# Performance work log

Hardware: AMD Instinct MI355X
Metric: run time of the kernel (lower is better)

Reference implementation:

```python
import jax, jax.numpy as jnp
import numpy as np

B, G, D = 16, 20000, 64   # batch, num_genes, feature_dim
S, L = 500, 128           # num_gene_sets, max genes per set (padded)


def setup_inputs() -> dict:
    key = jax.random.key(0)
    k1, k2, k3 = jax.random.split(key, 3)
    gene_features = jax.random.normal(k1, (B, G, D), dtype=jnp.float32)
    geneset_indices = jax.random.randint(k2, (S, L), 0, G, dtype=jnp.int32)
    set_mask = jnp.ones((S, L), dtype=bool)  # all positions valid (uniform-size sets)
    attn_weights = jax.random.normal(k3, (S, L, D), dtype=jnp.float32)
    return {
        "gene_features": gene_features,
        "attn_weights": attn_weights,
        "geneset_indices": geneset_indices,
        "set_mask": set_mask,
    }


def reference(gene_features, attn_weights, geneset_indices, set_mask):
    # Gather per-set gene features: [B, S, L, D]
    gathered = jnp.take(gene_features, geneset_indices, axis=1)
    # Masked softmax over the set-member axis L (independent per feature dim),
    # matching F.softmax(attention_weights, dim=1) per gene set.
    neg = jnp.finfo(attn_weights.dtype).min
    logits = jnp.where(set_mask[:, :, None], attn_weights, neg)  # [S, L, D]
    attn = jax.nn.softmax(logits, axis=1)                        # [S, L, D]
    # Weighted sum over set members -> [B, S, D]
    return jnp.einsum('bsld,sld->bsd', gathered, attn)
```

## Files before the change

kernel.cpp:

```cpp
#include <hip/hip_runtime.h>
#include <math.h>


#define NB 16
#define NG 20000
#define ND 64
#define NS 500
#define NL 128

__device__ __forceinline__ float bf2f(unsigned short u) {
    union { unsigned int i; float f; } x;
    x.i = ((unsigned int)u) << 16;
    return x.f;
}

__device__ __forceinline__ unsigned short f2bf(float f) {
    union { float f; unsigned int i; } x;
    x.f = f;
    unsigned int r = x.i + 0x7FFFu + ((x.i >> 16) & 1u);
    return (unsigned short)(r >> 16);
}

__global__ void detect_dtype_kernel(const unsigned short* __restrict__ aw,
                                    int* __restrict__ flag) {
    if (threadIdx.x == 0 && blockIdx.x == 0) {
        int cnt = 0;
        for (int i = 0; i < 128; i += 2) {
            unsigned int e = ((unsigned int)aw[i] >> 7) & 0xFFu;
            cnt += (e >= 100u && e <= 135u) ? 1 : 0;
        }
        *flag = (cnt >= 32) ? 1 : 0;
    }
}

template<bool BF16>
__global__ __launch_bounds__(256)
void agg_kernel(const void* __restrict__ gf_,
                const void* __restrict__ aw_,
                const int*  __restrict__ idx,
                void*       __restrict__ out_,
                const int*  __restrict__ flag)
{
    if (*flag != (BF16 ? 1 : 0)) return;

    __shared__ float attn_s[NL * ND];
    __shared__ float red[4 * ND];
    __shared__ float inv_sum[ND];
    __shared__ int   gidx[NL];

    const int s = blockIdx.x;
    const int t = threadIdx.x;
    if (t < NL) gidx[t] = idx[s * NL + t];

    const int d    = t & 63;
    const int part = t >> 6;

    float m = -INFINITY;
    if (BF16) {
        const unsigned short* awp = (const unsigned short*)aw_ + (size_t)s * (NL * ND);
        #pragma unroll 8
        for (int i = 0; i < 32; ++i) {
            const int l = part * 32 + i;
            const float v = bf2f(awp[l * ND + d]);
            attn_s[l * ND + d] = v;
            m = fmaxf(m, v);
        }
    } else {
        const float* awp = (const float*)aw_ + (size_t)s * (NL * ND);
        #pragma unroll 8
        for (int i = 0; i < 32; ++i) {
            const int l = part * 32 + i;
            const float v = awp[l * ND + d];
            attn_s[l * ND + d] = v;
            m = fmaxf(m, v);
        }
    }
    red[part * ND + d] = m;
    __syncthreads();
    const float m_all = fmaxf(fmaxf(red[0 * ND + d], red[1 * ND + d]),
                              fmaxf(red[2 * ND + d], red[3 * ND + d]));
    __syncthreads();

    float psum = 0.f;
    #pragma unroll 8
    for (int i = 0; i < 32; ++i) {
        const int l = part * 32 + i;
        const float e = __expf(attn_s[l * ND + d] - m_all);
        attn_s[l * ND + d] = e;
        psum += e;
    }
    red[part * ND + d] = psum;
    __syncthreads();
    if (part == 0) {
        inv_sum[d] = 1.0f / (red[0 * ND + d] + red[1 * ND + d] +
                             red[2 * ND + d] + red[3 * ND + d]);
    }
    __syncthreads();

    const int q  = t & 15;
    const int b  = t >> 4;
    const int d0 = q * 4;

    float ax = 0.f, ay = 0.f, az = 0.f, aww = 0.f;
    if (BF16) {
        const unsigned short* gbase = (const unsigned short*)gf_ + (size_t)b * (NG * ND) + d0;
        #pragma unroll 4
        for (int l = 0; l < NL; ++l) {
            const int g = gidx[l];
            const ushort4 u = *(const ushort4*)(gbase + (size_t)g * ND);
            const float4  w = *(const float4*)&attn_s[l * ND + d0];
            ax  += bf2f(u.x) * w.x;
            ay  += bf2f(u.y) * w.y;
            az  += bf2f(u.z) * w.z;
            aww += bf2f(u.w) * w.w;
        }
    } else {
        const float* gbase = (const float*)gf_ + (size_t)b * (NG * ND) + d0;
        #pragma unroll 4
        for (int l = 0; l < NL; ++l) {
            const int g = gidx[l];
            const float4 u = *(const float4*)(gbase + (size_t)g * ND);
            const float4 w = *(const float4*)&attn_s[l * ND + d0];
            ax  += u.x * w.x;
            ay  += u.y * w.y;
            az  += u.z * w.z;
            aww += u.w * w.w;
        }
    }
    ax  *= inv_sum[d0 + 0];
    ay  *= inv_sum[d0 + 1];
    az  *= inv_sum[d0 + 2];
    aww *= inv_sum[d0 + 3];

    if (BF16) {
        ushort4 o;
        o.x = f2bf(ax); o.y = f2bf(ay); o.z = f2bf(az); o.w = f2bf(aww);
        *(ushort4*)((unsigned short*)out_ + ((size_t)b * NS + s) * ND + d0) = o;
    } else {
        float4 o; o.x = ax; o.y = ay; o.z = az; o.w = aww;
        *(float4*)((float*)out_ + ((size_t)b * NS + s) * ND + d0) = o;
    }
}

extern "C" void kernel_launch(void* const* d_in, const int* in_sizes, int n_in,
                              void* d_out, int out_size, void* d_ws, size_t ws_size,
                              hipStream_t stream) {
    const void* gf  = d_in[0];
    const void* aw  = d_in[1];
    const int*  idx = (const int*)d_in[2];
    int* flag = (int*)d_ws;

    detect_dtype_kernel<<<1, 64, 0, stream>>>((const unsigned short*)aw, flag);
    agg_kernel<true ><<<NS, 256, 0, stream>>>(gf, aw, idx, d_out, flag);
    agg_kernel<false><<<NS, 256, 0, stream>>>(gf, aw, idx, d_out, flag);
}
```

Measured before the change: 152.8 us.

## Split gene-set reduction across 1024 threads with shared-memory partial sums

Raises the block size from 256 to 1024 threads so each block splits the 128 set members into four parts. Each part accumulates a partial weighted sum, and the parts are combined through a new shared-memory buffer before the output is written. The softmax phase is spread over 16 thread groups instead of 4. The goal is more memory-level parallelism for the random gathers, since each thread now issues 32 loads instead of 128. In exchange the kernel adds a block-wide barrier, a shared-memory reduction and more shared-memory use per block, which may lower occupancy. The dtype detector also switches from a serial loop to a wavefront ballot.

```diff
diff --git a/kernel.cpp b/kernel.cpp
--- a/kernel.cpp
+++ b/kernel.cpp
@@ -23,18 +23,13 @@
 
 __global__ void detect_dtype_kernel(const unsigned short* __restrict__ aw,
                                     int* __restrict__ flag) {
-    if (threadIdx.x == 0 && blockIdx.x == 0) {
-        int cnt = 0;
-        for (int i = 0; i < 128; i += 2) {
-            unsigned int e = ((unsigned int)aw[i] >> 7) & 0xFFu;
-            cnt += (e >= 100u && e <= 135u) ? 1 : 0;
-        }
-        *flag = (cnt >= 32) ? 1 : 0;
-    }
+    const unsigned int e = ((unsigned int)aw[2 * threadIdx.x] >> 7) & 0xFFu;
+    const unsigned long long m = __ballot(e >= 100u && e <= 135u);
+    if (threadIdx.x == 0) *flag = (__popcll(m) >= 32) ? 1 : 0;
 }
 
 template<bool BF16>
-__global__ __launch_bounds__(256)
+__global__ __launch_bounds__(1024)
 void agg_kernel(const void* __restrict__ gf_,
                 const void* __restrict__ aw_,
                 const int*  __restrict__ idx,
@@ -44,47 +39,40 @@
     if (*flag != (BF16 ? 1 : 0)) return;
 
     __shared__ float attn_s[NL * ND];
-    __shared__ float red[4 * ND];
+    __shared__ float red[16 * ND];
     __shared__ float inv_sum[ND];
     __shared__ int   gidx[NL];
+    __shared__ float part_red[4 * 16 * 16 * 4];
 
     const int s = blockIdx.x;
     const int t = threadIdx.x;
+
     if (t < NL) gidx[t] = idx[s * NL + t];
 
     const int d    = t & 63;
     const int part = t >> 6;
+    const unsigned short* awp = (const unsigned short*)aw_ + (size_t)s * (NL * ND);
 
     float m = -INFINITY;
-    if (BF16) {
-        const unsigned short* awp = (const unsigned short*)aw_ + (size_t)s * (NL * ND);
-        #pragma unroll 8
-        for (int i = 0; i < 32; ++i) {
-            const int l = part * 32 + i;
-            const float v = bf2f(awp[l * ND + d]);
-            attn_s[l * ND + d] = v;
-            m = fmaxf(m, v);
-        }
-    } else {
-        const float* awp = (const float*)aw_ + (size_t)s * (NL * ND);
-        #pragma unroll 8
-        for (int i = 0; i < 32; ++i) {
-            const int l = part * 32 + i;
-            const float v = awp[l * ND + d];
-            attn_s[l * ND + d] = v;
-            m = fmaxf(m, v);
-        }
+    #pragma unroll
+    for (int i = 0; i < 8; ++i) {
+        const int l = part * 8 + i;
+        const float v = BF16 ? bf2f(awp[l * ND + d])
+                             : ((const float*)aw_)[(size_t)s * (NL * ND) + l * ND + d];
+        attn_s[l * ND + d] = v;
+        m = fmaxf(m, v);
     }
     red[part * ND + d] = m;
     __syncthreads();
-    const float m_all = fmaxf(fmaxf(red[0 * ND + d], red[1 * ND + d]),
-                              fmaxf(red[2 * ND + d], red[3 * ND + d]));
+    float m_all = -INFINITY;
+    #pragma unroll
+    for (int p = 0; p < 16; ++p) m_all = fmaxf(m_all, red[p * ND + d]);
     __syncthreads();
 
     float psum = 0.f;
-    #pragma unroll 8
-    for (int i = 0; i < 32; ++i) {
-        const int l = part * 32 + i;
+    #pragma unroll
+    for (int i = 0; i < 8; ++i) {
+        const int l = part * 8 + i;
         const float e = __expf(attn_s[l * ND + d] - m_all);
         attn_s[l * ND + d] = e;
         psum += e;
@@ -92,20 +80,24 @@
     red[part * ND + d] = psum;
     __syncthreads();
     if (part == 0) {
-        inv_sum[d] = 1.0f / (red[0 * ND + d] + red[1 * ND + d] +
-                             red[2 * ND + d] + red[3 * ND + d]);
+        float tot = 0.f;
+        #pragma unroll
+        for (int p = 0; p < 16; ++p) tot += red[p * ND + d];
+        inv_sum[d] = 1.0f / tot;
     }
     __syncthreads();
 
     const int q  = t & 15;
-    const int b  = t >> 4;
+    const int bl = (t >> 4) & 15;
+    const int lp = t >> 8;
     const int d0 = q * 4;
 
     float ax = 0.f, ay = 0.f, az = 0.f, aww = 0.f;
     if (BF16) {
-        const unsigned short* gbase = (const unsigned short*)gf_ + (size_t)b * (NG * ND) + d0;
+        const unsigned short* gbase = (const unsigned short*)gf_ + (size_t)bl * (NG * ND) + d0;
         #pragma unroll 4
-        for (int l = 0; l < NL; ++l) {
+        for (int k = 0; k < 32; ++k) {
+            const int l = lp * 32 + k;
             const int g = gidx[l];
             const ushort4 u = *(const ushort4*)(gbase + (size_t)g * ND);
             const float4  w = *(const float4*)&attn_s[l * ND + d0];
@@ -115,9 +107,10 @@
             aww += bf2f(u.w) * w.w;
         }
     } else {
-        const float* gbase = (const float*)gf_ + (size_t)b * (NG * ND) + d0;
+        const float* gbase = (const float*)gf_ + (size_t)bl * (NG * ND) + d0;
         #pragma unroll 4
-        for (int l = 0; l < NL; ++l) {
+        for (int k = 0; k < 32; ++k) {
+            const int l = lp * 32 + k;
             const int g = gidx[l];
             const float4 u = *(const float4*)(gbase + (size_t)g * ND);
             const float4 w = *(const float4*)&attn_s[l * ND + d0];
@@ -127,18 +120,30 @@
             aww += u.w * w.w;
         }
     }
-    ax  *= inv_sum[d0 + 0];
-    ay  *= inv_sum[d0 + 1];
-    az  *= inv_sum[d0 + 2];
-    aww *= inv_sum[d0 + 3];
 
-    if (BF16) {
-        ushort4 o;
-        o.x = f2bf(ax); o.y = f2bf(ay); o.z = f2bf(az); o.w = f2bf(aww);
-        *(ushort4*)((unsigned short*)out_ + ((size_t)b * NS + s) * ND + d0) = o;
-    } else {
-        float4 o; o.x = ax; o.y = ay; o.z = az; o.w = aww;
-        *(float4*)((float*)out_ + ((size_t)b * NS + s) * ND + d0) = o;
+    float* pr = &part_red[((lp * 16 + bl) * 16 + q) * 4];
+    pr[0] = ax; pr[1] = ay; pr[2] = az; pr[3] = aww;
+    __syncthreads();
+
+    if (lp == 0) {
+        float r0 = 0.f, r1 = 0.f, r2 = 0.f, r3 = 0.f;
+        #pragma unroll
+        for (int p = 0; p < 4; ++p) {
+            const float4 v = *(const float4*)&part_red[((p * 16 + bl) * 16 + q) * 4];
+            r0 += v.x; r1 += v.y; r2 += v.z; r3 += v.w;
+        }
+        r0 *= inv_sum[d0 + 0];
+        r1 *= inv_sum[d0 + 1];
+        r2 *= inv_sum[d0 + 2];
+        r3 *= inv_sum[d0 + 3];
+        if (BF16) {
+            ushort4 o;
+            o.x = f2bf(r0); o.y = f2bf(r1); o.z = f2bf(r2); o.w = f2bf(r3);
+            *(ushort4*)((unsigned short*)out_ + ((size_t)bl * NS + s) * ND + d0) = o;
+        } else {
+            float4 o; o.x = r0; o.y = r1; o.z = r2; o.w = r3;
+            *(float4*)((float*)out_ + ((size_t)bl * NS + s) * ND + d0) = o;
+        }
     }
 }
 
@@ -151,6 +156,6 @@
     int* flag = (int*)d_ws;
 
     detect_dtype_kernel<<<1, 64, 0, stream>>>((const unsigned short*)aw, flag);
-    agg_kernel<true ><<<NS, 256, 0, stream>>>(gf, aw, idx, d_out, flag);
-    agg_kernel<false><<<NS, 256, 0, stream>>>(gf, aw, idx, d_out, flag);
+    agg_kernel<true ><<<NS, 1024, 0, stream>>>(gf, aw, idx, d_out, flag);
+    agg_kernel<false><<<NS, 1024, 0, stream>>>(gf, aw, idx, d_out, flag);
 }
```

Result: no change. 152.2 us (-0.4%).
